# Optimization experiments

Measured on AMD Instinct MI355X. Metric: run time of the kernel, lower is better.

## Reference

```python
import jax, jax.numpy as jnp
import numpy as np

N = 100_000
E = 1_600_000
IN_DIM = 128
PE_DIM = 16
HID = 128
LAT = 64
K = 4  # Chebyshev order


def _prop(w_hat, src, dst, x):
    # y[i] = sum_{e: dst[e]=i} w_hat[e] * x[src[e]]  (sparse matvec with L_hat)
    return jnp.zeros_like(x).at[dst].add(w_hat[:, None] * x[src])


def _cheb_layer(x, w_hat, src, dst, W, b):
    # PyG ChebConv with sym normalization, lambda_max=2: L_hat = -D^{-1/2} A D^{-1/2}
    # Tx0 = x; Tx1 = L_hat x; Tx_k = 2 L_hat Tx_{k-1} - Tx_{k-2}; out = sum_k Tx_k @ W_k + b
    Tx0 = x
    out = Tx0 @ W[0]
    Tx1 = _prop(w_hat, src, dst, x)
    out = out + Tx1 @ W[1]
    for k in range(2, K):
        Tx2 = 2.0 * _prop(w_hat, src, dst, Tx1) - Tx0
        out = out + Tx2 @ W[k]
        Tx0, Tx1 = Tx1, Tx2
    return out + b


def setup_inputs() -> dict:
    key = jax.random.key(0)
    ks = jax.random.split(key, 8)
    x = jax.random.normal(ks[0], (N, IN_DIM), jnp.float32)
    lap_pe = jax.random.normal(ks[1], (N, PE_DIM), jnp.float32)
    edge_index = jax.random.randint(ks[2], (2, E), 0, N)
    edge_weight = jax.random.uniform(ks[3], (E,), jnp.float32)
    d0 = IN_DIM + PE_DIM
    W0 = jax.random.normal(ks[4], (K, d0, HID), jnp.float32) / np.float32(np.sqrt(d0))
    b0 = jnp.zeros((HID,), jnp.float32)
    W1 = jax.random.normal(ks[5], (K, HID, HID), jnp.float32) / np.float32(np.sqrt(HID))
    b1 = jnp.zeros((HID,), jnp.float32)
    Wmu = jax.random.normal(ks[6], (HID, LAT), jnp.float32) / np.float32(np.sqrt(HID))
    bmu = jnp.zeros((LAT,), jnp.float32)
    Wlv = jax.random.normal(ks[7], (HID, LAT), jnp.float32) / np.float32(np.sqrt(HID))
    blv = jnp.zeros((LAT,), jnp.float32)
    return dict(x=x, edge_index=edge_index, lap_pe=lap_pe, edge_weight=edge_weight,
                W0=W0, b0=b0, W1=W1, b1=b1, Wmu=Wmu, bmu=bmu, Wlv=Wlv, blv=blv)


def reference(x, edge_index, lap_pe, edge_weight, W0, b0, W1, b1, Wmu, bmu, Wlv, blv):
    src, dst = edge_index[0], edge_index[1]
    # Encoder adds self-loops, ChebConv removes them before get_laplacian -> net: drop self-loops
    w = jnp.where(src == dst, jnp.zeros((), x.dtype), edge_weight)
    deg = jnp.zeros((x.shape[0],), x.dtype).at[src].add(w)
    deg_safe = jnp.where(deg > 0, deg, jnp.ones((), x.dtype))
    dis = jnp.where(deg > 0, jax.lax.rsqrt(deg_safe), jnp.zeros((), x.dtype))
    w_hat = -dis[src] * w * dis[dst]  # scaled Laplacian off-diagonal; diagonal = 0

    h = jnp.concatenate([x, lap_pe], axis=1)  # [N, in_dim + pe_dim]
    h = jax.nn.relu(_cheb_layer(h, w_hat, src, dst, W0, b0))
    h = jax.nn.relu(_cheb_layer(h, w_hat, src, dst, W1, b1))
    mu = h @ Wmu + bmu
    logvar = h @ Wlv + blv
    return (mu, logvar)
```

## Files before the change

### kernel.cpp

```cpp
#include <hip/hip_runtime.h>
#include <hip/hip_bf16.h>

typedef float f32x4 __attribute__((ext_vector_type(4)));
typedef unsigned short u16x8 __attribute__((ext_vector_type(8)));

static __device__ __forceinline__ void mfma16(f32x4& c, const u16x8& a, const u16x8& b) {
    asm("v_mfma_f32_16x16x32_bf16 %0, %1, %2, %0" : "+v"(c) : "v"(a), "v"(b));
}

static __device__ __forceinline__ unsigned short f2bf(float f) {
    __hip_bfloat16 h = __float2bfloat16(f);
    return *reinterpret_cast<unsigned short*>(&h);
}

static __device__ __forceinline__ float bflo(unsigned int v) { return __uint_as_float(v << 16); }
static __device__ __forceinline__ float bfhi(unsigned int v) { return __uint_as_float(v & 0xffff0000u); }


__global__ __launch_bounds__(1024) void k_dis_blocksum(float* deg, const int* __restrict__ cnt,
                                                       int* bsum, int N) {
    __shared__ int sd[1024];
    int i = blockIdx.x * 1024 + threadIdx.x;
    if (i < N) {
        float d = deg[i];
        deg[i] = (d > 0.f) ? rsqrtf(d) : 0.f;
    }
    sd[threadIdx.x] = (i < N) ? cnt[i] : 0;
    __syncthreads();
    for (int s = 512; s > 0; s >>= 1) {
        if (threadIdx.x < s) sd[threadIdx.x] += sd[threadIdx.x + s];
        __syncthreads();
    }
    if (threadIdx.x == 0) bsum[blockIdx.x] = sd[0];
}

__global__ __launch_bounds__(128) void k_scan_bsum(int* bsum, int nb) {
    __shared__ int sd[128];
    int t = threadIdx.x;
    int v = (t < nb) ? bsum[t] : 0;
    sd[t] = v;
    __syncthreads();
    for (int d = 1; d < 128; d <<= 1) {
        int x = (t >= d) ? sd[t - d] : 0;
        __syncthreads();
        sd[t] += x;
        __syncthreads();
    }
    if (t < nb) bsum[t] = sd[t] - v;
}

__global__ __launch_bounds__(1024) void k_scan(const int* __restrict__ cnt, const int* __restrict__ bsum,
                                               int* rowp, int N) {
    __shared__ int sd[1024];
    int i = blockIdx.x * 1024 + threadIdx.x;
    int v = (i < N) ? cnt[i] : 0;
    sd[threadIdx.x] = v;
    __syncthreads();
    for (int d = 1; d < 1024; d <<= 1) {
        int x = (threadIdx.x >= d) ? sd[threadIdx.x - d] : 0;
        __syncthreads();
        sd[threadIdx.x] += x;
        __syncthreads();
    }
    if (i < N) rowp[i] = sd[threadIdx.x] - v + bsum[blockIdx.x];
}

__global__ __launch_bounds__(256) void k_build_csr(const int* __restrict__ src, const int* __restrict__ dst,
                                                   const float* __restrict__ ew, const float* __restrict__ dis,
                                                   const int* __restrict__ rowp,
                                                   const unsigned char* __restrict__ rank,
                                                   int2* __restrict__ pack, int E) {
    int base = blockIdx.x * 512 + threadIdx.x;
#pragma unroll
    for (int u = 0; u < 2; u++) {
        int e = base + u * 256;
        if (e < E) {
            int s = src[e], d = dst[e];
            float w = (s == d) ? 0.f : ew[e];
            float wh = -dis[s] * w * dis[d];
            int pos = rowp[d] + (int)rank[e];
            int2 p;
            p.x = s;
            p.y = __float_as_int(wh);
            pack[pos] = p;
        }
    }
}


__global__ __launch_bounds__(256) void k_combine(const float* __restrict__ W, unsigned short* __restrict__ AT,
                                                 int D, int KPAD) {
    int i = blockIdx.x * 256 + threadIdx.x;
    int tot = 4 * 128 * KPAD;
    if (i >= tot) return;
    int sel = i / (128 * KPAD);
    int rem = i - sel * 128 * KPAD;
    int n = rem / KPAD;
    int kk = rem - n * KPAD;
    float v = 0.f;
    if (kk < D) {
        if (sel == 0)      v = W[(0 * D + kk) * 128 + n] - W[(2 * D + kk) * 128 + n];
        else if (sel == 1) v = W[(1 * D + kk) * 128 + n] - 3.f * W[(3 * D + kk) * 128 + n];
        else if (sel == 2) v = 2.f * W[(2 * D + kk) * 128 + n];
        else               v = 4.f * W[(3 * D + kk) * 128 + n];
    }
    AT[i] = f2bf(v);
}

__global__ __launch_bounds__(256) void k_headsT(const float* __restrict__ Wmu, const float* __restrict__ Wlv,
                                                unsigned short* __restrict__ AT) {
    int i = blockIdx.x * 256 + threadIdx.x;
    if (i >= 128 * 128) return;
    int n = i >> 7, kk = i & 127;
    float v = (n < 64) ? Wmu[kk * 64 + n] : Wlv[kk * 64 + (n - 64)];
    AT[i] = f2bf(v);
}


template <int KPAD, int SRC>
static __device__ __forceinline__ void gemm_pair_regB(const unsigned short* __restrict__ Abf,
                                                      const float* __restrict__ x,
                                                      const float* __restrict__ pe,
                                                      const unsigned short* __restrict__ Bta,
                                                      const unsigned short* __restrict__ Btb,
                                                      unsigned short* __restrict__ outA,
                                                      unsigned short* __restrict__ outB,
                                                      int N, int bx, unsigned short* As) {
    constexpr int LP = KPAD + 8;
    const int tid = threadIdx.x;
    const int row0 = bx * 64;

    {
        constexpr int TOT = 64 * KPAD;
        for (int c = tid * 8; c < TOT; c += 256 * 8) {
            int r = c / KPAD;
            int k = c - r * KPAD;
            int gr = row0 + r;
            if (gr > N - 1) gr = N - 1;
            u16x8 v;
            if (SRC == 0) {
                v = *reinterpret_cast<const u16x8*>(&Abf[(size_t)gr * KPAD + k]);
            } else {
                if (k < 128) {
                    float4 f0 = *reinterpret_cast<const float4*>(&x[(size_t)gr * 128 + k]);
                    float4 f1 = *reinterpret_cast<const float4*>(&x[(size_t)gr * 128 + k + 4]);
                    v[0] = f2bf(f0.x); v[1] = f2bf(f0.y); v[2] = f2bf(f0.z); v[3] = f2bf(f0.w);
                    v[4] = f2bf(f1.x); v[5] = f2bf(f1.y); v[6] = f2bf(f1.z); v[7] = f2bf(f1.w);
                } else if (k < 144) {
                    float4 f0 = *reinterpret_cast<const float4*>(&pe[(size_t)gr * 16 + (k - 128)]);
                    float4 f1 = *reinterpret_cast<const float4*>(&pe[(size_t)gr * 16 + (k - 124)]);
                    v[0] = f2bf(f0.x); v[1] = f2bf(f0.y); v[2] = f2bf(f0.z); v[3] = f2bf(f0.w);
                    v[4] = f2bf(f1.x); v[5] = f2bf(f1.y); v[6] = f2bf(f1.z); v[7] = f2bf(f1.w);
                } else {
                    v = (u16x8){0, 0, 0, 0, 0, 0, 0, 0};
                }
            }
            *reinterpret_cast<u16x8*>(&As[r * LP + k]) = v;
        }
    }
    __syncthreads();

    const int wave = tid >> 6, lane = tid & 63;
    const int wm = wave & 1, ww = wave >> 1;
    const int lr = lane & 15, lg = lane >> 4;
    const unsigned short* Bw = ww ? Btb : Bta;

    f32x4 acc[2][8];
#pragma unroll
    for (int i = 0; i < 2; i++)
#pragma unroll
        for (int j = 0; j < 8; j++) acc[i][j] = (f32x4){0.f, 0.f, 0.f, 0.f};

    asm volatile("s_nop 7"
                 : "+v"(acc[0][0]), "+v"(acc[0][4]), "+v"(acc[1][0]), "+v"(acc[1][4]));

    constexpr int KS = KPAD / 32;
#pragma unroll
    for (int ks = 0; ks < KS; ks++) {
        u16x8 a0 = *reinterpret_cast<const u16x8*>(&As[(wm * 32 + lr) * LP + ks * 32 + lg * 8]);
        u16x8 a1 = *reinterpret_cast<const u16x8*>(&As[(wm * 32 + 16 + lr) * LP + ks * 32 + lg * 8]);
#pragma unroll
        for (int g = 0; g < 2; g++) {
            u16x8 b[4];
#pragma unroll
            for (int j = 0; j < 4; j++)
                b[j] = *reinterpret_cast<const u16x8*>(&Bw[(size_t)((g * 4 + j) * 16 + lr) * KPAD + ks * 32 + lg * 8]);
#pragma unroll
            for (int j = 0; j < 4; j++) {
                mfma16(acc[0][g * 4 + j], a0, b[j]);
                mfma16(acc[1][g * 4 + j], a1, b[j]);
            }
        }
    }

    asm volatile("s_nop 7\n\ts_nop 7\n\ts_nop 7"
                 : "+v"(acc[0][0]), "+v"(acc[0][4]), "+v"(acc[1][0]), "+v"(acc[1][4]));

    unsigned short* outp = ww ? outB : outA;
#pragma unroll
    for (int fm = 0; fm < 2; fm++)
#pragma unroll
        for (int fn = 0; fn < 8; fn++)
#pragma unroll
            for (int i = 0; i < 4; i++) {
                int r = row0 + wm * 32 + fm * 16 + lg * 4 + i;
                if (r < N) outp[(size_t)r * 128 + fn * 16 + lr] = f2bf(acc[fm][fn][i]);
            }
}

__global__ __launch_bounds__(256, 4) void k_gemm_pair128(const unsigned short* __restrict__ Abf,
                                                         const unsigned short* __restrict__ AT1,
                                                         unsigned short* __restrict__ oZ3,
                                                         unsigned short* __restrict__ oZ2,
                                                         unsigned short* __restrict__ oZ1,
                                                         unsigned short* __restrict__ oZ0,
                                                         int N) {
    __shared__ __align__(16) unsigned short As[64 * 136];
    const int P = blockIdx.y;
    const unsigned short* Bta = AT1 + (size_t)(3 - 2 * P) * 128 * 128;
    const unsigned short* Btb = AT1 + (size_t)(2 - 2 * P) * 128 * 128;
    unsigned short* outA = (P == 0) ? oZ3 : oZ1;
    unsigned short* outB = (P == 0) ? oZ2 : oZ0;
    gemm_pair_regB<128, 0>(Abf, nullptr, nullptr, Bta, Btb, outA, outB, N, blockIdx.x, As);
}


__global__ __launch_bounds__(256, 4) void k_mega(const int* __restrict__ src, const int* __restrict__ dst,
                                                 const float* __restrict__ ew,
                                                 float* deg, int* cnt, unsigned char* __restrict__ rank,
                                                 const float* __restrict__ x, const float* __restrict__ pe,
                                                 const unsigned short* __restrict__ AT0,
                                                 unsigned short* __restrict__ oZ3, unsigned short* __restrict__ oZ2,
                                                 unsigned short* __restrict__ oZ1, unsigned short* __restrict__ oZ0,
                                                 int N, int E, int EPC) {
    __shared__ __align__(16) unsigned short As[64 * 168];
    const int bid = blockIdx.x;

    {
        int P = bid & 1;
        int bx = bid >> 1;
        const unsigned short* Bta = AT0 + (size_t)(3 - 2 * P) * 128 * 160;
        const unsigned short* Btb = AT0 + (size_t)(2 - 2 * P) * 128 * 160;
        unsigned short* outA = (P == 0) ? oZ3 : oZ1;
        unsigned short* outB = (P == 0) ? oZ2 : oZ0;
        gemm_pair_regB<160, 1>(nullptr, x, pe, Bta, Btb, outA, outB, N, bx, As);
    }

    {
        int e0 = bid * EPC;
        int e1 = e0 + EPC;
        if (e1 > E) e1 = E;
        for (int e = e0 + threadIdx.x; e < e1; e += 256) {
            int s = src[e], d = dst[e];
            float w = (s == d) ? 0.f : ew[e];
            atomicAdd(&deg[s], w);
            rank[e] = (unsigned char)atomicAdd(&cnt[d], 1);
        }
    }
}


__global__ __launch_bounds__(256, 4) void k_gemm_heads(const unsigned short* __restrict__ Abf,
                                                       const unsigned short* __restrict__ Bt,
                                                       float* __restrict__ out,
                                                       const float* __restrict__ bmu, const float* __restrict__ blv,
                                                       int N) {
    constexpr int KPAD = 128;
    constexpr int LP = KPAD + 8;
    __shared__ __align__(16) unsigned short As[128 * LP];
    const int tid = threadIdx.x;
    const int row0 = blockIdx.x * 128;

    {
        constexpr int TOT = 128 * KPAD;
        for (int c = tid * 8; c < TOT; c += 256 * 8) {
            int r = c / KPAD;
            int k = c - r * KPAD;
            int gr = row0 + r;
            if (gr > N - 1) gr = N - 1;
            u16x8 v = *reinterpret_cast<const u16x8*>(&Abf[(size_t)gr * KPAD + k]);
            *reinterpret_cast<u16x8*>(&As[r * LP + k]) = v;
        }
    }
    __syncthreads();

    const int wave = tid >> 6, lane = tid & 63;
    const int lr = lane & 15, lg = lane >> 4;

    f32x4 acc[2][8];
#pragma unroll
    for (int i = 0; i < 2; i++)
#pragma unroll
        for (int j = 0; j < 8; j++) acc[i][j] = (f32x4){0.f, 0.f, 0.f, 0.f};

    asm volatile("s_nop 7"
                 : "+v"(acc[0][0]), "+v"(acc[0][4]), "+v"(acc[1][0]), "+v"(acc[1][4]));

#pragma unroll
    for (int ks = 0; ks < KPAD / 32; ks++) {
        u16x8 a0 = *reinterpret_cast<const u16x8*>(&As[(wave * 32 + lr) * LP + ks * 32 + lg * 8]);
        u16x8 a1 = *reinterpret_cast<const u16x8*>(&As[(wave * 32 + 16 + lr) * LP + ks * 32 + lg * 8]);
#pragma unroll
        for (int g = 0; g < 2; g++) {
            u16x8 b[4];
#pragma unroll
            for (int j = 0; j < 4; j++)
                b[j] = *reinterpret_cast<const u16x8*>(&Bt[(size_t)((g * 4 + j) * 16 + lr) * KPAD + ks * 32 + lg * 8]);
#pragma unroll
            for (int j = 0; j < 4; j++) {
                mfma16(acc[0][g * 4 + j], a0, b[j]);
                mfma16(acc[1][g * 4 + j], a1, b[j]);
            }
        }
    }

    asm volatile("s_nop 7\n\ts_nop 7\n\ts_nop 7"
                 : "+v"(acc[0][0]), "+v"(acc[0][4]), "+v"(acc[1][0]), "+v"(acc[1][4]));

#pragma unroll
    for (int fm = 0; fm < 2; fm++)
#pragma unroll
        for (int fn = 0; fn < 8; fn++)
#pragma unroll
            for (int i = 0; i < 4; i++) {
                int r = row0 + wave * 32 + fm * 16 + lg * 4 + i;
                if (r < N) {
                    int c = fn * 16 + lr;
                    if (c < 64) out[(size_t)r * 64 + c] = acc[fm][fn][i] + bmu[c];
                    else out[(size_t)N * 64 + (size_t)r * 64 + (c - 64)] = acc[fm][fn][i] + blv[c - 64];
                }
            }
}


template <int MODE>
__global__ __launch_bounds__(256) void k_prop(const uint4* __restrict__ tin4,
                                              const uint4* __restrict__ z4,
                                              uint4* __restrict__ tout4,
                                              const float* __restrict__ bias,
                                              const int* __restrict__ rowp,
                                              const long long* __restrict__ pack,
                                              int N, int E) {
    int wave = threadIdx.x >> 6, lane = threadIdx.x & 63;
    int node = blockIdx.x * 4 + wave;
    if (node >= N) return;
    int beg = rowp[node];
    int end = (node == N - 1) ? E : rowp[node + 1];
    const int grp = lane >> 4, li = lane & 15;
    float s0 = 0.f, s1 = 0.f, s2 = 0.f, s3 = 0.f, s4 = 0.f, s5 = 0.f, s6 = 0.f, s7 = 0.f;
    int e = beg + grp;
    for (; e + 4 < end; e += 8) {
        long long qa = __builtin_nontemporal_load(pack + e);
        long long qb = __builtin_nontemporal_load(pack + e + 4);
        uint4 va = tin4[(size_t)(unsigned int)qa * 16 + li];
        uint4 vb = tin4[(size_t)(unsigned int)qb * 16 + li];
        float wa = __uint_as_float((unsigned int)((unsigned long long)qa >> 32));
        float wb = __uint_as_float((unsigned int)((unsigned long long)qb >> 32));
        s0 = fmaf(wa, bflo(va.x), s0); s1 = fmaf(wa, bfhi(va.x), s1);
        s2 = fmaf(wa, bflo(va.y), s2); s3 = fmaf(wa, bfhi(va.y), s3);
        s4 = fmaf(wa, bflo(va.z), s4); s5 = fmaf(wa, bfhi(va.z), s5);
        s6 = fmaf(wa, bflo(va.w), s6); s7 = fmaf(wa, bfhi(va.w), s7);
        s0 = fmaf(wb, bflo(vb.x), s0); s1 = fmaf(wb, bfhi(vb.x), s1);
        s2 = fmaf(wb, bflo(vb.y), s2); s3 = fmaf(wb, bfhi(vb.y), s3);
        s4 = fmaf(wb, bflo(vb.z), s4); s5 = fmaf(wb, bfhi(vb.z), s5);
        s6 = fmaf(wb, bflo(vb.w), s6); s7 = fmaf(wb, bfhi(vb.w), s7);
    }
    for (; e < end; e += 4) {
        long long qa = __builtin_nontemporal_load(pack + e);
        uint4 va = tin4[(size_t)(unsigned int)qa * 16 + li];
        float wa = __uint_as_float((unsigned int)((unsigned long long)qa >> 32));
        s0 = fmaf(wa, bflo(va.x), s0); s1 = fmaf(wa, bfhi(va.x), s1);
        s2 = fmaf(wa, bflo(va.y), s2); s3 = fmaf(wa, bfhi(va.y), s3);
        s4 = fmaf(wa, bflo(va.z), s4); s5 = fmaf(wa, bfhi(va.z), s5);
        s6 = fmaf(wa, bflo(va.w), s6); s7 = fmaf(wa, bfhi(va.w), s7);
    }
    s0 += __shfl_xor(s0, 16); s1 += __shfl_xor(s1, 16);
    s2 += __shfl_xor(s2, 16); s3 += __shfl_xor(s3, 16);
    s4 += __shfl_xor(s4, 16); s5 += __shfl_xor(s5, 16);
    s6 += __shfl_xor(s6, 16); s7 += __shfl_xor(s7, 16);
    s0 += __shfl_xor(s0, 32); s1 += __shfl_xor(s1, 32);
    s2 += __shfl_xor(s2, 32); s3 += __shfl_xor(s3, 32);
    s4 += __shfl_xor(s4, 32); s5 += __shfl_xor(s5, 32);
    s6 += __shfl_xor(s6, 32); s7 += __shfl_xor(s7, 32);
    if (lane < 16) {
        uint4 zv = z4[(size_t)node * 16 + li];
        float r0 = bflo(zv.x) + s0, r1 = bfhi(zv.x) + s1;
        float r2 = bflo(zv.y) + s2, r3 = bfhi(zv.y) + s3;
        float r4 = bflo(zv.z) + s4, r5 = bfhi(zv.z) + s5;
        float r6 = bflo(zv.w) + s6, r7 = bfhi(zv.w) + s7;
        if (MODE == 1) {
            const float* bp = bias + li * 8;
            r0 = fmaxf(r0 + bp[0], 0.f); r1 = fmaxf(r1 + bp[1], 0.f);
            r2 = fmaxf(r2 + bp[2], 0.f); r3 = fmaxf(r3 + bp[3], 0.f);
            r4 = fmaxf(r4 + bp[4], 0.f); r5 = fmaxf(r5 + bp[5], 0.f);
            r6 = fmaxf(r6 + bp[6], 0.f); r7 = fmaxf(r7 + bp[7], 0.f);
        }
        uint4 o;
        o.x = (unsigned int)f2bf(r0) | ((unsigned int)f2bf(r1) << 16);
        o.y = (unsigned int)f2bf(r2) | ((unsigned int)f2bf(r3) << 16);
        o.z = (unsigned int)f2bf(r4) | ((unsigned int)f2bf(r5) << 16);
        o.w = (unsigned int)f2bf(r6) | ((unsigned int)f2bf(r7) << 16);
        tout4[(size_t)node * 16 + li] = o;
    }
}


extern "C" void kernel_launch(void* const* d_in, const int* in_sizes, int n_in,
                              void* d_out, int out_size, void* d_ws, size_t ws_size,
                              hipStream_t stream) {
    const float* x   = (const float*)d_in[0];
    const int*   ei  = (const int*)d_in[1];
    const float* pe  = (const float*)d_in[2];
    const float* ew  = (const float*)d_in[3];
    const float* W0  = (const float*)d_in[4];
    const float* b0  = (const float*)d_in[5];
    const float* W1  = (const float*)d_in[6];
    const float* b1  = (const float*)d_in[7];
    const float* Wmu = (const float*)d_in[8];
    const float* bmu = (const float*)d_in[9];
    const float* Wlv = (const float*)d_in[10];
    const float* blv = (const float*)d_in[11];

    const int N = in_sizes[0] / 128;
    const int E = in_sizes[3];
    const int* src = ei;
    const int* dst = ei + E;

    char* ws = (char*)d_ws;
    size_t off = 0;
    auto alloc = [&](size_t bytes) {
        size_t o = off;
        off += (bytes + 1023) & ~(size_t)1023;
        return o;
    };
    float* deg = (float*)(ws + alloc(4 * (size_t)N));
    int* cnt   = (int*)(ws + alloc(4 * (size_t)N));
    size_t zero_bytes = off;
    unsigned char* rank = (unsigned char*)(ws + alloc((size_t)E));
    int* rowp  = (int*)(ws + alloc(4 * (size_t)N));
    int* bsum  = (int*)(ws + alloc(4 * 128));
    unsigned short* AT0 = (unsigned short*)(ws + alloc(2 * 4 * 128 * 160));
    unsigned short* AT1 = (unsigned short*)(ws + alloc(2 * 4 * 128 * 128));
    unsigned short* ATH = (unsigned short*)(ws + alloc(2 * 128 * 128));
    int2* pack = (int2*)(ws + alloc(8 * (size_t)E));
    unsigned int* B1 = (unsigned int*)(ws + alloc(2 * (size_t)N * 128));
    unsigned int* B2 = (unsigned int*)(ws + alloc(2 * (size_t)N * 128));
    unsigned int* B3 = (unsigned int*)(ws + alloc(2 * (size_t)N * 128));
    unsigned int* B4 = (unsigned int*)(ws + alloc(2 * (size_t)N * 128));
    unsigned int* B5 = (unsigned int*)(ws + alloc(2 * (size_t)N * 128));

    hipMemsetAsync(ws, 0, zero_bytes, stream);

    dim3 b256(256);
    k_combine<<<dim3((4 * 128 * 160 + 255) / 256), b256, 0, stream>>>(W0, AT0, 144, 160);
    k_combine<<<dim3((4 * 128 * 128 + 255) / 256), b256, 0, stream>>>(W1, AT1, 128, 128);
    k_headsT<<<dim3((128 * 128 + 255) / 256), b256, 0, stream>>>(Wmu, Wlv, ATH);

    int G64 = (N + 63) / 64;
    int total = 2 * G64;
    int EPC = (E + total - 1) / total;
    k_mega<<<dim3(total), b256, 0, stream>>>(src, dst, ew, deg, cnt, rank, x, pe, AT0,
                                             (unsigned short*)B1, (unsigned short*)B2,
                                             (unsigned short*)B3, (unsigned short*)B4,
                                             N, E, EPC);

    int nb = (N + 1023) / 1024;
    k_dis_blocksum<<<dim3(nb), dim3(1024), 0, stream>>>(deg, cnt, bsum, N);
    k_scan_bsum<<<dim3(1), dim3(128), 0, stream>>>(bsum, nb);
    k_scan<<<dim3(nb), dim3(1024), 0, stream>>>(cnt, bsum, rowp, N);
    k_build_csr<<<dim3((E + 511) / 512), b256, 0, stream>>>(src, dst, ew, deg, rowp, rank, pack, E);

    dim3 gg(G64, 2);
    dim3 gh((N + 127) / 128);
    dim3 gp((N + 3) / 4);
    const long long* packll = (const long long*)pack;
    uint4* B1v = (uint4*)B1; uint4* B2v = (uint4*)B2; uint4* B3v = (uint4*)B3;
    uint4* B4v = (uint4*)B4; uint4* B5v = (uint4*)B5;

    k_prop<0><<<gp, b256, 0, stream>>>(B1v, B2v, B5v, nullptr, rowp, packll, N, E);
    k_prop<0><<<gp, b256, 0, stream>>>(B5v, B3v, B1v, nullptr, rowp, packll, N, E);
    k_prop<1><<<gp, b256, 0, stream>>>(B1v, B4v, B2v, b0, rowp, packll, N, E);

    const unsigned short* h1 = (const unsigned short*)B2;
    k_gemm_pair128<<<gg, b256, 0, stream>>>(h1, AT1,
                                            (unsigned short*)B3, (unsigned short*)B4,
                                            (unsigned short*)B1, (unsigned short*)B5, N);
    k_prop<0><<<gp, b256, 0, stream>>>(B3v, B4v, B2v, nullptr, rowp, packll, N, E);
    k_prop<0><<<gp, b256, 0, stream>>>(B2v, B1v, B3v, nullptr, rowp, packll, N, E);
    k_prop<1><<<gp, b256, 0, stream>>>(B3v, B5v, B4v, b1, rowp, packll, N, E);

    k_gemm_heads<<<gh, b256, 0, stream>>>((const unsigned short*)B4, ATH, (float*)d_out, bmu, blv, N);
}
```

Measured before the change: 766.2 us.

## Fuse layer-2 GEMM with heads and propagate before transforming in layer 2

Layer 2 now runs three plain propagations (U1=L h1, U2=L U1, U3=L U2) before any matmul, then a single fused kernel multiplies [h1,U1,U2,U3] by combined weights, applies bias and ReLU, and computes the mu/logvar heads from shared memory. This drops the separate pair GEMM and heads kernels and the intermediate h2 round trip. The propagation kernel also gives each wave two nodes so more gathers are in flight. The fused kernel reloads four A segments per tile, and the two-node loop adds divergence when the two nodes have different degrees.

```diff
diff --git a/kernel.cpp b/kernel.cpp
--- a/kernel.cpp
+++ b/kernel.cpp
@@ -117,9 +117,8 @@
 }
 
 
-template <int KPAD, int SRC>
-static __device__ __forceinline__ void gemm_pair_regB(const unsigned short* __restrict__ Abf,
-                                                      const float* __restrict__ x,
+template <int KPAD>
+static __device__ __forceinline__ void gemm_pair_regB(const float* __restrict__ x,
                                                       const float* __restrict__ pe,
                                                       const unsigned short* __restrict__ Bta,
                                                       const unsigned short* __restrict__ Btb,
@@ -138,22 +137,18 @@
             int gr = row0 + r;
             if (gr > N - 1) gr = N - 1;
             u16x8 v;
-            if (SRC == 0) {
-                v = *reinterpret_cast<const u16x8*>(&Abf[(size_t)gr * KPAD + k]);
+            if (k < 128) {
+                float4 f0 = *reinterpret_cast<const float4*>(&x[(size_t)gr * 128 + k]);
+                float4 f1 = *reinterpret_cast<const float4*>(&x[(size_t)gr * 128 + k + 4]);
+                v[0] = f2bf(f0.x); v[1] = f2bf(f0.y); v[2] = f2bf(f0.z); v[3] = f2bf(f0.w);
+                v[4] = f2bf(f1.x); v[5] = f2bf(f1.y); v[6] = f2bf(f1.z); v[7] = f2bf(f1.w);
+            } else if (k < 144) {
+                float4 f0 = *reinterpret_cast<const float4*>(&pe[(size_t)gr * 16 + (k - 128)]);
+                float4 f1 = *reinterpret_cast<const float4*>(&pe[(size_t)gr * 16 + (k - 124)]);
+                v[0] = f2bf(f0.x); v[1] = f2bf(f0.y); v[2] = f2bf(f0.z); v[3] = f2bf(f0.w);
+                v[4] = f2bf(f1.x); v[5] = f2bf(f1.y); v[6] = f2bf(f1.z); v[7] = f2bf(f1.w);
             } else {
-                if (k < 128) {
-                    float4 f0 = *reinterpret_cast<const float4*>(&x[(size_t)gr * 128 + k]);
-                    float4 f1 = *reinterpret_cast<const float4*>(&x[(size_t)gr * 128 + k + 4]);
-                    v[0] = f2bf(f0.x); v[1] = f2bf(f0.y); v[2] = f2bf(f0.z); v[3] = f2bf(f0.w);
-                    v[4] = f2bf(f1.x); v[5] = f2bf(f1.y); v[6] = f2bf(f1.z); v[7] = f2bf(f1.w);
-                } else if (k < 144) {
-                    float4 f0 = *reinterpret_cast<const float4*>(&pe[(size_t)gr * 16 + (k - 128)]);
-                    float4 f1 = *reinterpret_cast<const float4*>(&pe[(size_t)gr * 16 + (k - 124)]);
-                    v[0] = f2bf(f0.x); v[1] = f2bf(f0.y); v[2] = f2bf(f0.z); v[3] = f2bf(f0.w);
-                    v[4] = f2bf(f1.x); v[5] = f2bf(f1.y); v[6] = f2bf(f1.z); v[7] = f2bf(f1.w);
-                } else {
-                    v = (u16x8){0, 0, 0, 0, 0, 0, 0, 0};
-                }
+                v = (u16x8){0, 0, 0, 0, 0, 0, 0, 0};
             }
             *reinterpret_cast<u16x8*>(&As[r * LP + k]) = v;
         }
@@ -206,22 +201,6 @@
                 int r = row0 + wm * 32 + fm * 16 + lg * 4 + i;
                 if (r < N) outp[(size_t)r * 128 + fn * 16 + lr] = f2bf(acc[fm][fn][i]);
             }
-}
-
-__global__ __launch_bounds__(256, 4) void k_gemm_pair128(const unsigned short* __restrict__ Abf,
-                                                         const unsigned short* __restrict__ AT1,
-                                                         unsigned short* __restrict__ oZ3,
-                                                         unsigned short* __restrict__ oZ2,
-                                                         unsigned short* __restrict__ oZ1,
-                                                         unsigned short* __restrict__ oZ0,
-                                                         int N) {
-    __shared__ __align__(16) unsigned short As[64 * 136];
-    const int P = blockIdx.y;
-    const unsigned short* Bta = AT1 + (size_t)(3 - 2 * P) * 128 * 128;
-    const unsigned short* Btb = AT1 + (size_t)(2 - 2 * P) * 128 * 128;
-    unsigned short* outA = (P == 0) ? oZ3 : oZ1;
-    unsigned short* outB = (P == 0) ? oZ2 : oZ0;
-    gemm_pair_regB<128, 0>(Abf, nullptr, nullptr, Bta, Btb, outA, outB, N, blockIdx.x, As);
 }
 
 
@@ -243,7 +222,7 @@
         const unsigned short* Btb = AT0 + (size_t)(2 - 2 * P) * 128 * 160;
         unsigned short* outA = (P == 0) ? oZ3 : oZ1;
         unsigned short* outB = (P == 0) ? oZ2 : oZ0;
-        gemm_pair_regB<160, 1>(nullptr, x, pe, Bta, Btb, outA, outB, N, bx, As);
+        gemm_pair_regB<160>(x, pe, Bta, Btb, outA, outB, N, bx, As);
     }
 
     {
@@ -260,74 +239,115 @@
 }
 
 
-__global__ __launch_bounds__(256, 4) void k_gemm_heads(const unsigned short* __restrict__ Abf,
-                                                       const unsigned short* __restrict__ Bt,
-                                                       float* __restrict__ out,
-                                                       const float* __restrict__ bmu, const float* __restrict__ blv,
-                                                       int N) {
-    constexpr int KPAD = 128;
-    constexpr int LP = KPAD + 8;
-    __shared__ __align__(16) unsigned short As[128 * LP];
+__global__ __launch_bounds__(256, 4) void k_gemm_l1_heads(const unsigned short* __restrict__ h1,
+                                                          const unsigned short* __restrict__ U1,
+                                                          const unsigned short* __restrict__ U2,
+                                                          const unsigned short* __restrict__ U3,
+                                                          const unsigned short* __restrict__ AT1,
+                                                          const unsigned short* __restrict__ ATH,
+                                                          const float* __restrict__ b1,
+                                                          const float* __restrict__ bmu,
+                                                          const float* __restrict__ blv,
+                                                          float* __restrict__ out, int N) {
+    constexpr int LP = 136;
+    __shared__ __align__(16) unsigned short As[64 * LP];
     const int tid = threadIdx.x;
-    const int row0 = blockIdx.x * 128;
-
-    {
-        constexpr int TOT = 128 * KPAD;
-        for (int c = tid * 8; c < TOT; c += 256 * 8) {
-            int r = c / KPAD;
-            int k = c - r * KPAD;
+    const int row0 = blockIdx.x * 64;
+    const int wave = tid >> 6, lane = tid & 63;
+    const int wm = wave & 1, wn = wave >> 1;
+    const int lr = lane & 15, lg = lane >> 4;
+
+    f32x4 acc[2][4];
+#pragma unroll
+    for (int i = 0; i < 2; i++)
+#pragma unroll
+        for (int j = 0; j < 4; j++) acc[i][j] = (f32x4){0.f, 0.f, 0.f, 0.f};
+
+#pragma unroll 4
+    for (int seg = 0; seg < 4; seg++) {
+        const unsigned short* sp = (seg == 0) ? h1 : (seg == 1) ? U1 : (seg == 2) ? U2 : U3;
+        for (int c = tid * 8; c < 64 * 128; c += 256 * 8) {
+            int r = c >> 7;
+            int k = c & 127;
             int gr = row0 + r;
             if (gr > N - 1) gr = N - 1;
-            u16x8 v = *reinterpret_cast<const u16x8*>(&Abf[(size_t)gr * KPAD + k]);
+            u16x8 v = *reinterpret_cast<const u16x8*>(&sp[(size_t)gr * 128 + k]);
             *reinterpret_cast<u16x8*>(&As[r * LP + k]) = v;
         }
-    }
+        __syncthreads();
+        const unsigned short* Bseg = AT1 + (size_t)seg * 128 * 128;
+#pragma unroll
+        for (int ks = 0; ks < 4; ks++) {
+            u16x8 a0 = *reinterpret_cast<const u16x8*>(&As[(wm * 32 + lr) * LP + ks * 32 + lg * 8]);
+            u16x8 a1 = *reinterpret_cast<const u16x8*>(&As[(wm * 32 + 16 + lr) * LP + ks * 32 + lg * 8]);
+            u16x8 b[4];
+#pragma unroll
+            for (int j = 0; j < 4; j++)
+                b[j] = *reinterpret_cast<const u16x8*>(&Bseg[(size_t)((wn * 64 + j * 16 + lr)) * 128 + ks * 32 + lg * 8]);
+#pragma unroll
+            for (int j = 0; j < 4; j++) {
+                mfma16(acc[0][j], a0, b[j]);
+                mfma16(acc[1][j], a1, b[j]);
+            }
+        }
+        __syncthreads();
+    }
+
+    asm volatile("s_nop 7\n\ts_nop 7\n\ts_nop 7"
+                 : "+v"(acc[0][0]), "+v"(acc[0][1]), "+v"(acc[0][2]), "+v"(acc[0][3]),
+                   "+v"(acc[1][0]), "+v"(acc[1][1]), "+v"(acc[1][2]), "+v"(acc[1][3]));
+
+#pragma unroll
+    for (int fm = 0; fm < 2; fm++)
+#pragma unroll
+        for (int fn = 0; fn < 4; fn++)
+#pragma unroll
+            for (int i = 0; i < 4; i++) {
+                int rl = wm * 32 + fm * 16 + lg * 4 + i;
+                int c = wn * 64 + fn * 16 + lr;
+                float v = fmaxf(acc[fm][fn][i] + b1[c], 0.f);
+                As[rl * LP + c] = f2bf(v);
+            }
     __syncthreads();
 
-    const int wave = tid >> 6, lane = tid & 63;
-    const int lr = lane & 15, lg = lane >> 4;
-
-    f32x4 acc[2][8];
+    f32x4 acc2[2][4];
 #pragma unroll
     for (int i = 0; i < 2; i++)
 #pragma unroll
-        for (int j = 0; j < 8; j++) acc[i][j] = (f32x4){0.f, 0.f, 0.f, 0.f};
+        for (int j = 0; j < 4; j++) acc2[i][j] = (f32x4){0.f, 0.f, 0.f, 0.f};
 
     asm volatile("s_nop 7"
-                 : "+v"(acc[0][0]), "+v"(acc[0][4]), "+v"(acc[1][0]), "+v"(acc[1][4]));
-
-#pragma unroll
-    for (int ks = 0; ks < KPAD / 32; ks++) {
-        u16x8 a0 = *reinterpret_cast<const u16x8*>(&As[(wave * 32 + lr) * LP + ks * 32 + lg * 8]);
-        u16x8 a1 = *reinterpret_cast<const u16x8*>(&As[(wave * 32 + 16 + lr) * LP + ks * 32 + lg * 8]);
-#pragma unroll
-        for (int g = 0; g < 2; g++) {
-            u16x8 b[4];
-#pragma unroll
-            for (int j = 0; j < 4; j++)
-                b[j] = *reinterpret_cast<const u16x8*>(&Bt[(size_t)((g * 4 + j) * 16 + lr) * KPAD + ks * 32 + lg * 8]);
-#pragma unroll
-            for (int j = 0; j < 4; j++) {
-                mfma16(acc[0][g * 4 + j], a0, b[j]);
-                mfma16(acc[1][g * 4 + j], a1, b[j]);
-            }
+                 : "+v"(acc2[0][0]), "+v"(acc2[0][1]), "+v"(acc2[1][0]), "+v"(acc2[1][1]));
+
+#pragma unroll
+    for (int ks = 0; ks < 4; ks++) {
+        u16x8 a0 = *reinterpret_cast<const u16x8*>(&As[(wm * 32 + lr) * LP + ks * 32 + lg * 8]);
+        u16x8 a1 = *reinterpret_cast<const u16x8*>(&As[(wm * 32 + 16 + lr) * LP + ks * 32 + lg * 8]);
+        u16x8 b[4];
+#pragma unroll
+        for (int j = 0; j < 4; j++)
+            b[j] = *reinterpret_cast<const u16x8*>(&ATH[(size_t)(wn * 64 + j * 16 + lr) * 128 + ks * 32 + lg * 8]);
+#pragma unroll
+        for (int j = 0; j < 4; j++) {
+            mfma16(acc2[0][j], a0, b[j]);
+            mfma16(acc2[1][j], a1, b[j]);
         }
     }
 
     asm volatile("s_nop 7\n\ts_nop 7\n\ts_nop 7"
-                 : "+v"(acc[0][0]), "+v"(acc[0][4]), "+v"(acc[1][0]), "+v"(acc[1][4]));
+                 : "+v"(acc2[0][0]), "+v"(acc2[0][1]), "+v"(acc2[1][0]), "+v"(acc2[1][1]));
 
 #pragma unroll
     for (int fm = 0; fm < 2; fm++)
 #pragma unroll
-        for (int fn = 0; fn < 8; fn++)
+        for (int fn = 0; fn < 4; fn++)
 #pragma unroll
             for (int i = 0; i < 4; i++) {
-                int r = row0 + wave * 32 + fm * 16 + lg * 4 + i;
+                int r = row0 + wm * 32 + fm * 16 + lg * 4 + i;
                 if (r < N) {
-                    int c = fn * 16 + lr;
-                    if (c < 64) out[(size_t)r * 64 + c] = acc[fm][fn][i] + bmu[c];
-                    else out[(size_t)N * 64 + (size_t)r * 64 + (c - 64)] = acc[fm][fn][i] + blv[c - 64];
+                    int c = wn * 64 + fn * 16 + lr;
+                    if (c < 64) out[(size_t)r * 64 + c] = acc2[fm][fn][i] + bmu[c];
+                    else out[(size_t)N * 64 + (size_t)r * 64 + (c - 64)] = acc2[fm][fn][i] + blv[c - 64];
                 }
             }
 }
@@ -342,52 +362,61 @@
                                               const long long* __restrict__ pack,
                                               int N, int E) {
     int wave = threadIdx.x >> 6, lane = threadIdx.x & 63;
-    int node = blockIdx.x * 4 + wave;
-    if (node >= N) return;
-    int beg = rowp[node];
-    int end = (node == N - 1) ? E : rowp[node + 1];
+    int n0 = blockIdx.x * 8 + wave * 2;
+    if (n0 >= N) return;
+    int n1 = n0 + 1;
     const int grp = lane >> 4, li = lane & 15;
+    int beg0 = rowp[n0];
+    int end0 = (n0 == N - 1) ? E : rowp[n0 + 1];
+    int beg1 = 0, end1 = 0;
+    if (n1 < N) {
+        beg1 = rowp[n1];
+        end1 = (n1 == N - 1) ? E : rowp[n1 + 1];
+    }
     float s0 = 0.f, s1 = 0.f, s2 = 0.f, s3 = 0.f, s4 = 0.f, s5 = 0.f, s6 = 0.f, s7 = 0.f;
-    int e = beg + grp;
-    for (; e + 4 < end; e += 8) {
-        long long qa = __builtin_nontemporal_load(pack + e);
-        long long qb = __builtin_nontemporal_load(pack + e + 4);
-        uint4 va = tin4[(size_t)(unsigned int)qa * 16 + li];
-        uint4 vb = tin4[(size_t)(unsigned int)qb * 16 + li];
-        float wa = __uint_as_float((unsigned int)((unsigned long long)qa >> 32));
-        float wb = __uint_as_float((unsigned int)((unsigned long long)qb >> 32));
-        s0 = fmaf(wa, bflo(va.x), s0); s1 = fmaf(wa, bfhi(va.x), s1);
-        s2 = fmaf(wa, bflo(va.y), s2); s3 = fmaf(wa, bfhi(va.y), s3);
-        s4 = fmaf(wa, bflo(va.z), s4); s5 = fmaf(wa, bfhi(va.z), s5);
-        s6 = fmaf(wa, bflo(va.w), s6); s7 = fmaf(wa, bfhi(va.w), s7);
-        s0 = fmaf(wb, bflo(vb.x), s0); s1 = fmaf(wb, bfhi(vb.x), s1);
-        s2 = fmaf(wb, bflo(vb.y), s2); s3 = fmaf(wb, bfhi(vb.y), s3);
-        s4 = fmaf(wb, bflo(vb.z), s4); s5 = fmaf(wb, bfhi(vb.z), s5);
-        s6 = fmaf(wb, bflo(vb.w), s6); s7 = fmaf(wb, bfhi(vb.w), s7);
-    }
-    for (; e < end; e += 4) {
-        long long qa = __builtin_nontemporal_load(pack + e);
-        uint4 va = tin4[(size_t)(unsigned int)qa * 16 + li];
-        float wa = __uint_as_float((unsigned int)((unsigned long long)qa >> 32));
-        s0 = fmaf(wa, bflo(va.x), s0); s1 = fmaf(wa, bfhi(va.x), s1);
-        s2 = fmaf(wa, bflo(va.y), s2); s3 = fmaf(wa, bfhi(va.y), s3);
-        s4 = fmaf(wa, bflo(va.z), s4); s5 = fmaf(wa, bfhi(va.z), s5);
-        s6 = fmaf(wa, bflo(va.w), s6); s7 = fmaf(wa, bfhi(va.w), s7);
-    }
-    s0 += __shfl_xor(s0, 16); s1 += __shfl_xor(s1, 16);
-    s2 += __shfl_xor(s2, 16); s3 += __shfl_xor(s3, 16);
-    s4 += __shfl_xor(s4, 16); s5 += __shfl_xor(s5, 16);
-    s6 += __shfl_xor(s6, 16); s7 += __shfl_xor(s7, 16);
-    s0 += __shfl_xor(s0, 32); s1 += __shfl_xor(s1, 32);
-    s2 += __shfl_xor(s2, 32); s3 += __shfl_xor(s3, 32);
-    s4 += __shfl_xor(s4, 32); s5 += __shfl_xor(s5, 32);
-    s6 += __shfl_xor(s6, 32); s7 += __shfl_xor(s7, 32);
+    float t0 = 0.f, t1 = 0.f, t2 = 0.f, t3 = 0.f, t4 = 0.f, t5 = 0.f, t6 = 0.f, t7 = 0.f;
+    int e0 = beg0 + grp, e1 = beg1 + grp;
+    while (e0 < end0 || e1 < end1) {
+        bool p0 = e0 < end0, p1 = e1 < end1;
+        long long qa = 0, qb = 0;
+        uint4 va, vb;
+        if (p0) qa = __builtin_nontemporal_load(pack + e0);
+        if (p1) qb = __builtin_nontemporal_load(pack + e1);
+        if (p0) va = tin4[(size_t)(unsigned int)qa * 16 + li];
+        if (p1) vb = tin4[(size_t)(unsigned int)qb * 16 + li];
+        if (p0) {
+            float wa = __uint_as_float((unsigned int)((unsigned long long)qa >> 32));
+            s0 = fmaf(wa, bflo(va.x), s0); s1 = fmaf(wa, bfhi(va.x), s1);
+            s2 = fmaf(wa, bflo(va.y), s2); s3 = fmaf(wa, bfhi(va.y), s3);
+            s4 = fmaf(wa, bflo(va.z), s4); s5 = fmaf(wa, bfhi(va.z), s5);
+            s6 = fmaf(wa, bflo(va.w), s6); s7 = fmaf(wa, bfhi(va.w), s7);
+        }
+        if (p1) {
+            float wb = __uint_as_float((unsigned int)((unsigned long long)qb >> 32));
+            t0 = fmaf(wb, bflo(vb.x), t0); t1 = fmaf(wb, bfhi(vb.x), t1);
+            t2 = fmaf(wb, bflo(vb.y), t2); t3 = fmaf(wb, bfhi(vb.y), t3);
+            t4 = fmaf(wb, bflo(vb.z), t4); t5 = fmaf(wb, bfhi(vb.z), t5);
+            t6 = fmaf(wb, bflo(vb.w), t6); t7 = fmaf(wb, bfhi(vb.w), t7);
+        }
+        e0 += 4;
+        e1 += 4;
+    }
+    s0 += __shfl_xor(s0, 16); s1 += __shfl_xor(s1, 16); s2 += __shfl_xor(s2, 16); s3 += __shfl_xor(s3, 16);
+    s4 += __shfl_xor(s4, 16); s5 += __shfl_xor(s5, 16); s6 += __shfl_xor(s6, 16); s7 += __shfl_xor(s7, 16);
+    s0 += __shfl_xor(s0, 32); s1 += __shfl_xor(s1, 32); s2 += __shfl_xor(s2, 32); s3 += __shfl_xor(s3, 32);
+    s4 += __shfl_xor(s4, 32); s5 += __shfl_xor(s5, 32); s6 += __shfl_xor(s6, 32); s7 += __shfl_xor(s7, 32);
+    t0 += __shfl_xor(t0, 16); t1 += __shfl_xor(t1, 16); t2 += __shfl_xor(t2, 16); t3 += __shfl_xor(t3, 16);
+    t4 += __shfl_xor(t4, 16); t5 += __shfl_xor(t5, 16); t6 += __shfl_xor(t6, 16); t7 += __shfl_xor(t7, 16);
+    t0 += __shfl_xor(t0, 32); t1 += __shfl_xor(t1, 32); t2 += __shfl_xor(t2, 32); t3 += __shfl_xor(t3, 32);
+    t4 += __shfl_xor(t4, 32); t5 += __shfl_xor(t5, 32); t6 += __shfl_xor(t6, 32); t7 += __shfl_xor(t7, 32);
+
     if (lane < 16) {
-        uint4 zv = z4[(size_t)node * 16 + li];
-        float r0 = bflo(zv.x) + s0, r1 = bfhi(zv.x) + s1;
-        float r2 = bflo(zv.y) + s2, r3 = bfhi(zv.y) + s3;
-        float r4 = bflo(zv.z) + s4, r5 = bfhi(zv.z) + s5;
-        float r6 = bflo(zv.w) + s6, r7 = bfhi(zv.w) + s7;
+        float r0 = s0, r1 = s1, r2 = s2, r3 = s3, r4 = s4, r5 = s5, r6 = s6, r7 = s7;
+        if (MODE != 2) {
+            uint4 zv = z4[(size_t)n0 * 16 + li];
+            r0 += bflo(zv.x); r1 += bfhi(zv.x); r2 += bflo(zv.y); r3 += bfhi(zv.y);
+            r4 += bflo(zv.z); r5 += bfhi(zv.z); r6 += bflo(zv.w); r7 += bfhi(zv.w);
+        }
         if (MODE == 1) {
             const float* bp = bias + li * 8;
             r0 = fmaxf(r0 + bp[0], 0.f); r1 = fmaxf(r1 + bp[1], 0.f);
@@ -400,7 +429,28 @@
         o.y = (unsigned int)f2bf(r2) | ((unsigned int)f2bf(r3) << 16);
         o.z = (unsigned int)f2bf(r4) | ((unsigned int)f2bf(r5) << 16);
         o.w = (unsigned int)f2bf(r6) | ((unsigned int)f2bf(r7) << 16);
-        tout4[(size_t)node * 16 + li] = o;
+        tout4[(size_t)n0 * 16 + li] = o;
+        if (n1 < N) {
+            float u0 = t0, u1 = t1, u2 = t2, u3 = t3, u4 = t4, u5 = t5, u6 = t6, u7 = t7;
+            if (MODE != 2) {
+                uint4 zv = z4[(size_t)n1 * 16 + li];
+                u0 += bflo(zv.x); u1 += bfhi(zv.x); u2 += bflo(zv.y); u3 += bfhi(zv.y);
+                u4 += bflo(zv.z); u5 += bfhi(zv.z); u6 += bflo(zv.w); u7 += bfhi(zv.w);
+            }
+            if (MODE == 1) {
+                const float* bp = bias + li * 8;
+                u0 = fmaxf(u0 + bp[0], 0.f); u1 = fmaxf(u1 + bp[1], 0.f);
+                u2 = fmaxf(u2 + bp[2], 0.f); u3 = fmaxf(u3 + bp[3], 0.f);
+                u4 = fmaxf(u4 + bp[4], 0.f); u5 = fmaxf(u5 + bp[5], 0.f);
+                u6 = fmaxf(u6 + bp[6], 0.f); u7 = fmaxf(u7 + bp[7], 0.f);
+            }
+            uint4 o2;
+            o2.x = (unsigned int)f2bf(u0) | ((unsigned int)f2bf(u1) << 16);
+            o2.y = (unsigned int)f2bf(u2) | ((unsigned int)f2bf(u3) << 16);
+            o2.z = (unsigned int)f2bf(u4) | ((unsigned int)f2bf(u5) << 16);
+            o2.w = (unsigned int)f2bf(u6) | ((unsigned int)f2bf(u7) << 16);
+            tout4[(size_t)n1 * 16 + li] = o2;
+        }
     }
 }
 
@@ -470,9 +520,7 @@
     k_scan<<<dim3(nb), dim3(1024), 0, stream>>>(cnt, bsum, rowp, N);
     k_build_csr<<<dim3((E + 511) / 512), b256, 0, stream>>>(src, dst, ew, deg, rowp, rank, pack, E);
 
-    dim3 gg(G64, 2);
-    dim3 gh((N + 127) / 128);
-    dim3 gp((N + 3) / 4);
+    dim3 gp((N + 7) / 8);
     const long long* packll = (const long long*)pack;
     uint4* B1v = (uint4*)B1; uint4* B2v = (uint4*)B2; uint4* B3v = (uint4*)B3;
     uint4* B4v = (uint4*)B4; uint4* B5v = (uint4*)B5;
@@ -481,13 +529,11 @@
     k_prop<0><<<gp, b256, 0, stream>>>(B5v, B3v, B1v, nullptr, rowp, packll, N, E);
     k_prop<1><<<gp, b256, 0, stream>>>(B1v, B4v, B2v, b0, rowp, packll, N, E);
 
-    const unsigned short* h1 = (const unsigned short*)B2;
-    k_gemm_pair128<<<gg, b256, 0, stream>>>(h1, AT1,
-                                            (unsigned short*)B3, (unsigned short*)B4,
-                                            (unsigned short*)B1, (unsigned short*)B5, N);
-    k_prop<0><<<gp, b256, 0, stream>>>(B3v, B4v, B2v, nullptr, rowp, packll, N, E);
-    k_prop<0><<<gp, b256, 0, stream>>>(B2v, B1v, B3v, nullptr, rowp, packll, N, E);
-    k_prop<1><<<gp, b256, 0, stream>>>(B3v, B5v, B4v, b1, rowp, packll, N, E);
-
-    k_gemm_heads<<<gh, b256, 0, stream>>>((const unsigned short*)B4, ATH, (float*)d_out, bmu, blv, N);
-}
+    k_prop<2><<<gp, b256, 0, stream>>>(B2v, nullptr, B3v, nullptr, rowp, packll, N, E);
+    k_prop<2><<<gp, b256, 0, stream>>>(B3v, nullptr, B4v, nullptr, rowp, packll, N, E);
+    k_prop<2><<<gp, b256, 0, stream>>>(B4v, nullptr, B5v, nullptr, rowp, packll, N, E);
+
+    k_gemm_l1_heads<<<dim3(G64), b256, 0, stream>>>((const unsigned short*)B2, (const unsigned short*)B3,
+                                                    (const unsigned short*)B4, (const unsigned short*)B5,
+                                                    AT1, ATH, b1, bmu, blv, (float*)d_out, N);
+}
```

Measured after the change: 769.7 us. No clear change (+0.4%).
